# Optimization experiments

Hardware: AMD Instinct MI355X
Metric: run time of the kernel (lower is better)

Reference implementation:

```python
import jax, jax.numpy as jnp
import numpy as np

DIM = 1024
HEADS = 16
HEAD_DIM = DIM // HEADS
EPS = 1e-5


def setup_inputs() -> dict:
    key = jax.random.key(0)
    ks = jax.random.split(key, 4)
    N, L = 4, 2048
    x = jax.random.normal(ks[0], (N, L, DIM), dtype=jnp.float32)
    # causal mask: True means masked (strictly upper triangle)
    attn_mask = jnp.triu(jnp.ones((L, L), dtype=jnp.bool_), k=1)[None, None, :, :]
    w_qkv = jax.random.normal(ks[1], (3 * DIM, DIM), dtype=jnp.float32) * (DIM ** -0.5)
    w_proj = jax.random.normal(ks[2], (DIM, DIM), dtype=jnp.float32) * (DIM ** -0.5)
    b_proj = jnp.zeros((DIM,), dtype=jnp.float32)
    q_gamma = jnp.ones((HEAD_DIM,), dtype=jnp.float32)
    q_beta = jnp.zeros((HEAD_DIM,), dtype=jnp.float32)
    k_gamma = jnp.ones((HEAD_DIM,), dtype=jnp.float32)
    k_beta = jnp.zeros((HEAD_DIM,), dtype=jnp.float32)
    return {"x": x, "attn_mask": attn_mask, "w_qkv": w_qkv, "w_proj": w_proj,
            "b_proj": b_proj, "q_gamma": q_gamma, "q_beta": q_beta,
            "k_gamma": k_gamma, "k_beta": k_beta}


def _layernorm(h, gamma, beta):
    mu = jnp.mean(h, axis=-1, keepdims=True)
    var = jnp.mean(jnp.square(h - mu), axis=-1, keepdims=True)
    return (h - mu) * jax.lax.rsqrt(var + EPS) * gamma + beta


def reference(x, attn_mask, w_qkv, w_proj, b_proj, q_gamma, q_beta, k_gamma, k_beta):
    N, L, D = x.shape
    H, hd = HEADS, HEAD_DIM
    scale = hd ** -0.5
    qkv = jnp.einsum('nld,ed->nle', x, w_qkv)  # [N, L, 3D]
    qkv = qkv.reshape(N, L, 3, H, hd).transpose(2, 0, 3, 1, 4)  # [3, N, H, L, hd]
    q, k, v = qkv[0], qkv[1], qkv[2]
    q = _layernorm(q, q_gamma, q_beta)
    k = _layernorm(k, k_gamma, k_beta)
    scores = jnp.einsum('nhqd,nhkd->nhqk', q * scale, k)
    scores = scores + jnp.where(attn_mask, -jnp.inf, 0.0).astype(scores.dtype)
    attn = jax.nn.softmax(scores, axis=-1)
    out = jnp.einsum('nhqk,nhkd->nhqd', attn, v)  # [N, H, L, hd]
    out = out.transpose(0, 2, 1, 3).reshape(N, L, D)
    return jnp.einsum('nld,ed->nle', out, w_proj) + b_proj
```

## Files before the change

kernel.cpp:

```cpp
#include <hip/hip_runtime.h>


using f16x8 = __attribute__((ext_vector_type(8))) _Float16;
using f16x4 = __attribute__((ext_vector_type(4))) _Float16;
using f16x2 = __attribute__((ext_vector_type(2))) _Float16;
using f32x4 = __attribute__((ext_vector_type(4))) float;
using f32x16 = __attribute__((ext_vector_type(16))) float;
using u32x4 = __attribute__((ext_vector_type(4))) unsigned int;

#define MFMA16(a, b, c) __builtin_amdgcn_mfma_f32_16x16x32_f16(a, b, c, 0, 0, 0)
#define MFMA32(a, b, c) __builtin_amdgcn_mfma_f32_32x32x16_f16(a, b, c, 0, 0, 0)

__device__ __forceinline__ void gload_lds16(const void* g, void* l) {
  __builtin_amdgcn_global_load_lds(
      (const __attribute__((address_space(1))) unsigned int*)g,
      (__attribute__((address_space(3))) unsigned int*)l, 16, 0, 0);
}

__device__ __forceinline__ float dot2acc(unsigned int pk, float c) {
#if __has_builtin(__builtin_amdgcn_fdot2)
  const f16x2 ones = {(_Float16)1.f, (_Float16)1.f};
  return __builtin_amdgcn_fdot2(__builtin_bit_cast(f16x2, pk), ones, c, false);
#else
  f16x2 v = __builtin_bit_cast(f16x2, pk);
  return c + (float)v[0] + (float)v[1];
#endif
}

__global__ __launch_bounds__(256) void f32_to_f16_kernel(
    const float* __restrict__ in, _Float16* __restrict__ out, int n) {
  int i = (blockIdx.x * 256 + threadIdx.x) * 8;
  if (i >= n) return;
  float4 a = *(const float4*)(in + i);
  float4 b = *(const float4*)(in + i + 4);
  f16x8 o;
  o[0] = (_Float16)a.x; o[1] = (_Float16)a.y; o[2] = (_Float16)a.z; o[3] = (_Float16)a.w;
  o[4] = (_Float16)b.x; o[5] = (_Float16)b.y; o[6] = (_Float16)b.z; o[7] = (_Float16)b.w;
  *(f16x8*)(out + i) = o;
}

template <int MODE>
__global__ __launch_bounds__(256, 2) void gemm_bt(
    const _Float16* __restrict__ A, const _Float16* __restrict__ B,
    void* __restrict__ Cout, const float* __restrict__ bias,
    const float* __restrict__ qg, const float* __restrict__ qb,
    const float* __restrict__ kg, const float* __restrict__ kb,
    int M, int N, int K) {
  __shared__ __align__(16) _Float16 As[2][128 * 32];
  __shared__ __align__(16) _Float16 Bs[2][256 * 32];
  const int tid = threadIdx.x;
  const int w = tid >> 6, lane = tid & 63;
  const int c = lane & 15, g = lane >> 4;
  const long mbase = (long)blockIdx.x * 128;
  const long nbase = (long)blockIdx.y * 256;
  const int wm = (w >> 1) * 64, wn = (w & 1) * 128;
  const int sr4 = lane >> 2;
  const int scol = ((lane & 3) ^ ((lane >> 3) & 3)) * 8;
  const int sg = (g ^ ((c >> 1) & 3)) * 8;
  const char* pAr = (const char*)As + (wm + c) * 64 + sg * 2;
  const char* pBr = (const char*)Bs + (wn + c) * 64 + sg * 2;

#define GSTAGE(buf, kt_)                                                      \
  {                                                                           \
    const int kk_ = (kt_) * 32;                                               \
    _Pragma("unroll") for (int i = 0; i < 2; ++i) {                           \
      const int arow = w * 32 + i * 16 + sr4;                                 \
      gload_lds16(A + (mbase + arow) * K + kk_ + scol,                        \
                  &As[buf][(w * 2 + i) * 512]);                               \
    }                                                                         \
    _Pragma("unroll") for (int j = 0; j < 4; ++j) {                           \
      const int brow = w * 64 + j * 16 + sr4;                                 \
      gload_lds16(B + (nbase + brow) * K + kk_ + scol,                        \
                  &Bs[buf][(w * 4 + j) * 512]);                               \
    }                                                                         \
  }

#define GPHASE(BUF, t_)                                                       \
  {                                                                           \
    if ((t_) + 1 < nk) {                                                      \
      asm volatile("s_waitcnt vmcnt(6)" ::: "memory");                        \
    } else {                                                                  \
      asm volatile("s_waitcnt vmcnt(0)" ::: "memory");                        \
    }                                                                         \
    __builtin_amdgcn_sched_barrier(0);                                        \
    __builtin_amdgcn_s_barrier();                                             \
    __builtin_amdgcn_sched_barrier(0);                                        \
    f16x8 af[4], bfr[8];                                                      \
    _Pragma("unroll") for (int mt = 0; mt < 4; ++mt)                          \
        af[mt] = *(const f16x8*)(pAr + (BUF) * 8192 + mt * 1024);             \
    _Pragma("unroll") for (int nt = 0; nt < 8; ++nt)                          \
        bfr[nt] = *(const f16x8*)(pBr + (BUF) * 16384 + nt * 1024);           \
    asm volatile("s_waitcnt lgkmcnt(0)" ::: "memory");                        \
    __builtin_amdgcn_sched_barrier(0);                                        \
    __builtin_amdgcn_s_barrier();                                             \
    __builtin_amdgcn_sched_barrier(0);                                        \
    if ((t_) + 2 < nk) GSTAGE(BUF, (t_) + 2);                                 \
    __builtin_amdgcn_s_setprio(1);                                            \
    _Pragma("unroll") for (int mt = 0; mt < 4; ++mt)                          \
        _Pragma("unroll") for (int nt = 0; nt < 8; ++nt)                      \
            acc[mt][nt] = MFMA16(af[mt], bfr[nt], acc[mt][nt]);               \
    __builtin_amdgcn_s_setprio(0);                                            \
  }

  f32x4 acc[4][8];
#pragma unroll
  for (int i = 0; i < 4; ++i)
#pragma unroll
    for (int j = 0; j < 8; ++j) acc[i][j] = f32x4{0.f, 0.f, 0.f, 0.f};

  const int nk = K >> 5;
  GSTAGE(0, 0);
  GSTAGE(1, 1);
  for (int kt = 0; kt < nk; kt += 2) {
    GPHASE(0, kt);
    GPHASE(1, kt + 1);
  }
#undef GPHASE
#undef GSTAGE

  if constexpr (MODE == 1) {
    const int region = (int)(nbase >> 10);
    if (region < 2) {
      const float* gamma = region ? kg : qg;
      const float* beta = region ? kb : qb;
      float gam[4], bet[4];
#pragma unroll
      for (int j = 0; j < 4; ++j) {
        gam[j] = gamma[j * 16 + c];
        bet[j] = beta[j * 16 + c];
      }
      const float sc = region ? 1.f : 0.1803368801111204f;
#pragma unroll
      for (int mt = 0; mt < 4; ++mt)
#pragma unroll
        for (int hh = 0; hh < 2; ++hh)
#pragma unroll
          for (int r = 0; r < 4; ++r) {
            float s1 = 0.f, s2 = 0.f;
#pragma unroll
            for (int j = 0; j < 4; ++j) {
              const float v = acc[mt][hh * 4 + j][r];
              s1 += v;
              s2 += v * v;
            }
#pragma unroll
            for (int msk = 1; msk < 16; msk <<= 1) {
              s1 += __shfl_xor(s1, msk);
              s2 += __shfl_xor(s2, msk);
            }
            const float mu = s1 * 0.015625f;
            const float rstd = rsqrtf(s2 * 0.015625f - mu * mu + 1e-5f);
#pragma unroll
            for (int j = 0; j < 4; ++j)
              acc[mt][hh * 4 + j][r] =
                  ((acc[mt][hh * 4 + j][r] - mu) * rstd * gam[j] + bet[j]) * sc;
          }
    }
#pragma unroll
    for (int nt = 0; nt < 8; ++nt) {
      const long col = nbase + wn + nt * 16 + c;
#pragma unroll
      for (int mt = 0; mt < 4; ++mt)
#pragma unroll
        for (int r = 0; r < 4; ++r) {
          const long row = mbase + wm + mt * 16 + g * 4 + r;
          ((_Float16*)Cout)[row * N + col] = (_Float16)acc[mt][nt][r];
        }
    }
  } else {
#pragma unroll
    for (int nt = 0; nt < 8; ++nt) {
      const long col = nbase + wn + nt * 16 + c;
      const float bv = bias ? bias[col] : 0.f;
#pragma unroll
      for (int mt = 0; mt < 4; ++mt)
#pragma unroll
        for (int r = 0; r < 4; ++r) {
          const long row = mbase + wm + mt * 16 + g * 4 + r;
          ((float*)Cout)[row * N + col] = acc[mt][nt][r] + bv;
        }
    }
  }
}

__global__ __launch_bounds__(256) void transpose_v_kernel(
    const _Float16* __restrict__ qkv, _Float16* __restrict__ Vt) {
  __shared__ __align__(16) _Float16 tile[64][80];
  const int nh = blockIdx.y;
  const long n = nh >> 4;
  const int h = nh & 15;
  const long lbase = (long)blockIdx.x * 64;
  const int t = threadIdx.x;
#pragma unroll
  for (int r = 0; r < 2; ++r) {
    const int l = (t + r * 256) >> 3;
    const int cc = (t & 7) * 8;
    f16x8 v = *(const f16x8*)(qkv + (n * 2048 + lbase + l) * 3072 + 2048 + h * 64 + cc);
    *(f16x8*)&tile[l][cc] = v;
  }
  __syncthreads();
  const int d = t >> 2, q = t & 3;
  f16x8 o0, o1;
#pragma unroll
  for (int i = 0; i < 8; ++i) {
    o0[i] = tile[q * 16 + i][d];
    o1[i] = tile[q * 16 + 8 + i][d];
  }
  _Float16* dst = Vt + ((long)nh * 64 + d) * 2048 + lbase + q * 16;
  *(f16x8*)dst = o0;
  *(f16x8*)(dst + 8) = o1;
}

__global__ __launch_bounds__(256, 4) void attn_kernel(
    const _Float16* __restrict__ qkv, const _Float16* __restrict__ Vt,
    _Float16* __restrict__ Ob) {
  __shared__ __align__(16) char lds[32768];
  const int w = threadIdx.x >> 6;
  const int lane = threadIdx.x & 63;
  const int c5 = lane & 31;
  const int hi = lane >> 5;
  const int nh = blockIdx.x;
  const long n = nh >> 4;
  const int h = nh & 15;
  const int qtile = 15 - blockIdx.y;
  const int qlo_blk = qtile * 128;
  const int qlo = qlo_blk + w * 32;
  const int qrow = qlo + c5;

  const _Float16* Qp = qkv + n * 2048 * 3072 + h * 64;
  const _Float16* Kq = Qp + 1024;
  const _Float16* Vp = Vt + (long)nh * 64 * 2048;

  const int sr8 = lane >> 3;
  const int scol = ((lane & 7) ^ sr8) * 8;

  const int nkv_blk = (qlo_blk + 191) >> 6;
  const int nkv_w = (qlo + 95) >> 6;

#define STAGE(BUF, kv_)                                                        \
  {                                                                            \
    const int kb_ = (kv_) * 64;                                                \
    _Pragma("unroll") for (int i = 0; i < 2; ++i) {                            \
      const int idx = w * 2 + i;                                               \
      const int row = idx * 8 + sr8;                                           \
      gload_lds16(Kq + (long)(kb_ + row) * 3072 + scol,                        \
                  lds + (BUF) * 8192 + idx * 1024);                            \
      gload_lds16(Vp + (long)row * 2048 + kb_ + scol,                          \
                  lds + 16384 + (BUF) * 8192 + idx * 1024);                    \
    }                                                                          \
  }

  f16x8 qf[4];
#pragma unroll
  for (int dc = 0; dc < 4; ++dc)
    qf[dc] = *(const f16x8*)(Qp + (long)qrow * 3072 + dc * 16 + hi * 8);

  f32x16 negM;
#pragma unroll
  for (int r = 0; r < 16; ++r) negM[r] = -12.0f;

  f32x16 acc[2];
#pragma unroll
  for (int db = 0; db < 2; ++db)
#pragma unroll
    for (int r = 0; r < 16; ++r) acc[db][r] = 0.f;
  float ls = 0.f;

  const int swr = c5 & 7;
  const char* Lb[4];
#pragma unroll
  for (int j = 0; j < 4; ++j)
    Lb[j] = lds + c5 * 128 + (((j * 2 + hi) ^ swr) << 4);

#define COMPUTE(BUF, kv_)                                                      \
  {                                                                            \
    const int kbase = (kv_) * 64;                                              \
    f32x16 s0, s1;                                                             \
    __builtin_amdgcn_s_setprio(1);                                             \
    {                                                                          \
      f16x8 kf0 = *(const f16x8*)(Lb[0] + (BUF) * 8192);                       \
      f16x8 kf1 = *(const f16x8*)(Lb[0] + (BUF) * 8192 + 4096);                \
      s0 = MFMA32(kf0, qf[0], negM);                                           \
      s1 = MFMA32(kf1, qf[0], negM);                                           \
    }                                                                          \
    _Pragma("unroll") for (int dc = 1; dc < 4; ++dc) {                         \
      f16x8 kf0 = *(const f16x8*)(Lb[dc] + (BUF) * 8192);                      \
      f16x8 kf1 = *(const f16x8*)(Lb[dc] + (BUF) * 8192 + 4096);               \
      s0 = MFMA32(kf0, qf[dc], s0);                                            \
      s1 = MFMA32(kf1, qf[dc], s1);                                            \
    }                                                                          \
    __builtin_amdgcn_s_setprio(0);                                             \
    if (kbase + 63 > qlo) {                                                    \
      _Pragma("unroll") for (int r = 0; r < 16; ++r) {                         \
        const int mv = (r & 3) + 8 * (r >> 2) + 4 * hi;                        \
        if (kbase + mv > qrow) s0[r] = -1e30f;                                 \
        if (kbase + 32 + mv > qrow) s1[r] = -1e30f;                            \
      }                                                                        \
    }                                                                          \
    _Pragma("unroll") for (int r = 0; r < 16; ++r) {                           \
      s0[r] = exp2f(s0[r]);                                                    \
      s1[r] = exp2f(s1[r]);                                                    \
    }                                                                          \
    unsigned int pk0[4][2], pk1[4][2];                                         \
    _Pragma("unroll") for (int r2 = 0; r2 < 4; ++r2)                           \
        _Pragma("unroll") for (int p = 0; p < 2; ++p) {                        \
      pk0[r2][p] = __builtin_bit_cast(                                         \
          unsigned int, __builtin_amdgcn_cvt_pkrtz(s0[4 * r2 + 2 * p],         \
                                                   s0[4 * r2 + 2 * p + 1]));   \
      pk1[r2][p] = __builtin_bit_cast(                                         \
          unsigned int, __builtin_amdgcn_cvt_pkrtz(s1[4 * r2 + 2 * p],         \
                                                   s1[4 * r2 + 2 * p + 1]));   \
    }                                                                          \
    _Pragma("unroll") for (int r2 = 0; r2 < 4; ++r2)                           \
        _Pragma("unroll") for (int p = 0; p < 2; ++p) {                        \
      ls = dot2acc(pk0[r2][p], ls);                                            \
      ls = dot2acc(pk1[r2][p], ls);                                            \
    }                                                                          \
    f16x8 pB[4];                                                               \
    _Pragma("unroll") for (int kk = 0; kk < 4; ++kk) {                         \
      const int rx = (kk & 1) * 2;                                             \
      unsigned int x0 = (kk < 2) ? pk0[rx][0] : pk1[rx][0];                    \
      unsigned int y0 = (kk < 2) ? pk0[rx + 1][0] : pk1[rx + 1][0];            \
      unsigned int x1 = (kk < 2) ? pk0[rx][1] : pk1[rx][1];                    \
      unsigned int y1 = (kk < 2) ? pk0[rx + 1][1] : pk1[rx + 1][1];            \
      asm("v_permlane32_swap_b32 %0, %1" : "+v"(x0), "+v"(y0));                \
      asm("v_permlane32_swap_b32 %0, %1" : "+v"(x1), "+v"(y1));                \
      pB[kk] = __builtin_bit_cast(f16x8, u32x4{x0, x1, y0, y1});               \
    }                                                                          \
    __builtin_amdgcn_s_setprio(1);                                             \
    _Pragma("unroll") for (int db = 0; db < 2; ++db)                           \
        _Pragma("unroll") for (int kk = 0; kk < 4; ++kk) {                     \
      f16x8 vf = *(const f16x8*)(Lb[kk] + 16384 + (BUF) * 8192 + db * 4096);   \
      acc[db] = MFMA32(vf, pB[kk], acc[db]);                                   \
    }                                                                          \
    __builtin_amdgcn_s_setprio(0);                                             \
  }

  STAGE(0, 0);
  for (int kv = 0; kv < nkv_blk; kv += 2) {
    __syncthreads();
    if (kv + 1 < nkv_blk) STAGE(1, kv + 1);
    if (kv < nkv_w) COMPUTE(0, kv);
    if (kv + 1 >= nkv_blk) break;
    __syncthreads();
    if (kv + 2 < nkv_blk) STAGE(0, kv + 2);
    if (kv + 1 < nkv_w) COMPUTE(1, kv + 1);
  }
#undef COMPUTE
#undef STAGE

  const float lsr = ls + __shfl_xor(ls, 32);
  const float inv = 1.f / lsr;
  _Float16* ob = Ob + ((long)(n * 2048) + qrow) * 1024 + h * 64 + 4 * hi;
#pragma unroll
  for (int db = 0; db < 2; ++db)
#pragma unroll
    for (int r2 = 0; r2 < 4; ++r2) {
      f16x4 o;
#pragma unroll
      for (int j = 0; j < 4; ++j)
        o[j] = (_Float16)(acc[db][4 * r2 + j] * inv);
      *(f16x4*)(ob + db * 32 + 8 * r2) = o;
    }
}

extern "C" void kernel_launch(void* const* d_in, const int* in_sizes, int n_in,
                              void* d_out, int out_size, void* d_ws, size_t ws_size,
                              hipStream_t stream) {
  const float* x = (const float*)d_in[0];
  const float* w_qkv = (const float*)d_in[2];
  const float* w_proj = (const float*)d_in[3];
  const float* b_proj = (const float*)d_in[4];
  const float* qg = (const float*)d_in[5];
  const float* qb = (const float*)d_in[6];
  const float* kg = (const float*)d_in[7];
  const float* kb = (const float*)d_in[8];

  char* ws = (char*)d_ws;
  _Float16* xb     = (_Float16*)(ws + 0);
  _Float16* wqkvb  = (_Float16*)(ws + 16777216);
  _Float16* wprojb = (_Float16*)(ws + 23068672);
  _Float16* qkvh   = (_Float16*)(ws + 25165824);
  _Float16* Vt     = (_Float16*)(ws + 75497472);
  _Float16* Ob     = xb;

  f32_to_f16_kernel<<<4096, 256, 0, stream>>>(x, xb, 8388608);
  f32_to_f16_kernel<<<1536, 256, 0, stream>>>(w_qkv, wqkvb, 3145728);
  f32_to_f16_kernel<<<512, 256, 0, stream>>>(w_proj, wprojb, 1048576);

  gemm_bt<1><<<dim3(64, 12), 256, 0, stream>>>(xb, wqkvb, qkvh, nullptr,
                                               qg, qb, kg, kb, 8192, 3072, 1024);
  transpose_v_kernel<<<dim3(32, 64), 256, 0, stream>>>(qkvh, Vt);
  attn_kernel<<<dim3(64, 16), 256, 0, stream>>>(qkvh, Vt, Ob);
  gemm_bt<0><<<dim3(64, 4), 256, 0, stream>>>(Ob, wprojb, d_out, b_proj,
                                              nullptr, nullptr, nullptr, nullptr,
                                              8192, 1024, 1024);
}
```

Baseline: 200.5 us.

## Use triple-buffered LDS in GEMM to drop the second barrier per k-step

```diff
diff --git a/kernel.cpp b/kernel.cpp
--- a/kernel.cpp
+++ b/kernel.cpp
@@ -46,8 +46,8 @@
     const float* __restrict__ qg, const float* __restrict__ qb,
     const float* __restrict__ kg, const float* __restrict__ kb,
     int M, int N, int K) {
-  __shared__ __align__(16) _Float16 As[2][128 * 32];
-  __shared__ __align__(16) _Float16 Bs[2][256 * 32];
+  __shared__ __align__(16) _Float16 As[3][128 * 32];
+  __shared__ __align__(16) _Float16 Bs[3][256 * 32];
   const int tid = threadIdx.x;
   const int w = tid >> 6, lane = tid & 63;
   const int c = lane & 15, g = lane >> 4;
@@ -60,48 +60,21 @@
   const char* pAr = (const char*)As + (wm + c) * 64 + sg * 2;
   const char* pBr = (const char*)Bs + (wn + c) * 64 + sg * 2;
 
-#define GSTAGE(buf, kt_)                                                      \
+#define GSTAGE(aOff_, bOff_, kt_)                                             \
   {                                                                           \
     const int kk_ = (kt_) * 32;                                               \
     _Pragma("unroll") for (int i = 0; i < 2; ++i) {                           \
       const int arow = w * 32 + i * 16 + sr4;                                 \
       gload_lds16(A + (mbase + arow) * K + kk_ + scol,                        \
-                  &As[buf][(w * 2 + i) * 512]);                               \
+                  (char*)As + (aOff_) + (w * 2 + i) * 1024);                  \
     }                                                                         \
     _Pragma("unroll") for (int j = 0; j < 4; ++j) {                           \
       const int brow = w * 64 + j * 16 + sr4;                                 \
       gload_lds16(B + (nbase + brow) * K + kk_ + scol,                        \
-                  &Bs[buf][(w * 4 + j) * 512]);                               \
+                  (char*)Bs + (bOff_) + (w * 4 + j) * 1024);                  \
     }                                                                         \
   }
 
-#define GPHASE(BUF, t_)                                                       \
-  {                                                                           \
-    if ((t_) + 1 < nk) {                                                      \
-      asm volatile("s_waitcnt vmcnt(6)" ::: "memory");                        \
-    } else {                                                                  \
-      asm volatile("s_waitcnt vmcnt(0)" ::: "memory");                        \
-    }                                                                         \
-    __builtin_amdgcn_sched_barrier(0);                                        \
-    __builtin_amdgcn_s_barrier();                                             \
-    __builtin_amdgcn_sched_barrier(0);                                        \
-    f16x8 af[4], bfr[8];                                                      \
-    _Pragma("unroll") for (int mt = 0; mt < 4; ++mt)                          \
-        af[mt] = *(const f16x8*)(pAr + (BUF) * 8192 + mt * 1024);             \
-    _Pragma("unroll") for (int nt = 0; nt < 8; ++nt)                          \
-        bfr[nt] = *(const f16x8*)(pBr + (BUF) * 16384 + nt * 1024);           \
-    asm volatile("s_waitcnt lgkmcnt(0)" ::: "memory");                        \
-    __builtin_amdgcn_sched_barrier(0);                                        \
-    __builtin_amdgcn_s_barrier();                                             \
-    __builtin_amdgcn_sched_barrier(0);                                        \
-    if ((t_) + 2 < nk) GSTAGE(BUF, (t_) + 2);                                 \
-    __builtin_amdgcn_s_setprio(1);                                            \
-    _Pragma("unroll") for (int mt = 0; mt < 4; ++mt)                          \
-        _Pragma("unroll") for (int nt = 0; nt < 8; ++nt)                      \
-            acc[mt][nt] = MFMA16(af[mt], bfr[nt], acc[mt][nt]);               \
-    __builtin_amdgcn_s_setprio(0);                                            \
-  }
-
   f32x4 acc[4][8];
 #pragma unroll
   for (int i = 0; i < 4; ++i)
@@ -109,13 +82,39 @@
     for (int j = 0; j < 8; ++j) acc[i][j] = f32x4{0.f, 0.f, 0.f, 0.f};
 
   const int nk = K >> 5;
-  GSTAGE(0, 0);
-  GSTAGE(1, 1);
-  for (int kt = 0; kt < nk; kt += 2) {
-    GPHASE(0, kt);
-    GPHASE(1, kt + 1);
-  }
-#undef GPHASE
+  GSTAGE(0, 0, 0);
+  GSTAGE(8192, 16384, 1);
+  int aR = 0, bR = 0;
+  int aS = 16384, bS = 32768;
+  for (int kt = 0; kt < nk; ++kt) {
+    if (kt + 1 < nk) {
+      asm volatile("s_waitcnt vmcnt(6)" ::: "memory");
+    } else {
+      asm volatile("s_waitcnt vmcnt(0)" ::: "memory");
+    }
+    __builtin_amdgcn_sched_barrier(0);
+    __builtin_amdgcn_s_barrier();
+    __builtin_amdgcn_sched_barrier(0);
+    f16x8 af[4], bfr[8];
+#pragma unroll
+    for (int mt = 0; mt < 4; ++mt)
+      af[mt] = *(const f16x8*)(pAr + aR + mt * 1024);
+#pragma unroll
+    for (int nt = 0; nt < 8; ++nt)
+      bfr[nt] = *(const f16x8*)(pBr + bR + nt * 1024);
+    if (kt + 2 < nk) GSTAGE(aS, bS, kt + 2);
+    __builtin_amdgcn_s_setprio(1);
+#pragma unroll
+    for (int mt = 0; mt < 4; ++mt)
+#pragma unroll
+      for (int nt = 0; nt < 8; ++nt)
+        acc[mt][nt] = MFMA16(af[mt], bfr[nt], acc[mt][nt]);
+    __builtin_amdgcn_s_setprio(0);
+    aR = (aR == 16384) ? 0 : aR + 8192;
+    bR = (bR == 32768) ? 0 : bR + 16384;
+    aS = (aS == 16384) ? 0 : aS + 8192;
+    bS = (bS == 32768) ? 0 : bS + 16384;
+  }
 #undef GSTAGE
 
   if constexpr (MODE == 1) {
```

Result: faster. 195.1 us (-2.7%).
